# Kernel optimization log

Hardware: AMD Instinct MI355X
Metric: run time of the kernel (lower is better)

The kernel has to match this reference:

```python
import jax, jax.numpy as jnp
import numpy as np


def setup_inputs() -> dict:
    key = jax.random.key(0)
    k1, k2, k3, k4, k5 = jax.random.split(key, 5)
    B, S, d_in, d_out, r = 4, 2048, 4096, 4096, 16
    x = jax.random.normal(k1, (B, S, d_in), dtype=jnp.float32)
    weight = jax.random.normal(k2, (d_out, d_in), dtype=jnp.float32) * 0.02
    bias = jax.random.normal(k3, (d_out,), dtype=jnp.float32) * 0.02
    lora_A = jax.random.normal(k4, (r, d_in), dtype=jnp.float32) * 0.02
    lora_B = jax.random.normal(k5, (d_out, r), dtype=jnp.float32) * 0.02
    return {"x": x, "weight": weight, "bias": bias, "lora_A": lora_A, "lora_B": lora_B}


def reference(x, weight, bias, lora_A, lora_B):
    # weight_delta = lora_B @ lora_A  -> [out, in]; adjusted = W + delta
    # out = x @ adjusted.T + bias  (F.linear semantics)
    adjusted = weight + lora_B @ lora_A  # [out, in]
    return jnp.einsum('bsi,oi->bso', x, adjusted) + bias
```

## Files before the change

### kernel.cpp

```cpp
#include <hip/hip_runtime.h>
#include <hip/hip_bf16.h>
#include <stdint.h>

typedef int   intx4  __attribute__((ext_vector_type(4)));
typedef float floatx4 __attribute__((ext_vector_type(4)));

#define BM  256
#define BN  256
#define BKB 128

__device__ __forceinline__ void gload_lds16(const void* g, void* l) {
    auto* gp = reinterpret_cast<const __attribute__((address_space(1))) uint32_t*>(
        reinterpret_cast<uintptr_t>(g));
    auto* lp = reinterpret_cast<__attribute__((address_space(3))) uint32_t*>(
        reinterpret_cast<uintptr_t>(l));
    __builtin_amdgcn_global_load_lds(gp, lp, 16, 0, 0);
}

__global__ void quant_fused(const float* __restrict__ x, const float* __restrict__ W,
                            const float* __restrict__ lA, const float* __restrict__ lB,
                            int8_t* __restrict__ xq, int8_t* __restrict__ wq,
                            float* __restrict__ sx, float* __restrict__ sw,
                            long Mrows, int N, int K, int r) {
    __shared__ float red[4][4];
    const int tid = threadIdx.x;
    const int wv  = tid >> 6;
    const long b = blockIdx.x;

    if (b < Mrows) {
        const long row = b;
        const float* xr = x + (size_t)row * K;
        float4 v[4];
        float am = 0.f;
#pragma unroll
        for (int i = 0; i < 4; ++i) {
            v[i] = ((const float4*)xr)[i * 256 + tid];
            am = fmaxf(am, fmaxf(fmaxf(fabsf(v[i].x), fabsf(v[i].y)),
                                 fmaxf(fabsf(v[i].z), fabsf(v[i].w))));
        }
#pragma unroll
        for (int off = 32; off; off >>= 1) am = fmaxf(am, __shfl_xor(am, off));
        if ((tid & 63) == 0) red[0][wv] = am;
        __syncthreads();
        am = fmaxf(fmaxf(red[0][0], red[0][1]), fmaxf(red[0][2], red[0][3]));
        const float inv = am > 0.f ? 127.0f / am : 0.f;
        if (tid == 0) sx[row] = am > 0.f ? am / 127.0f : 0.f;
        int8_t* dst = xq + (size_t)row * K;
#pragma unroll
        for (int i = 0; i < 4; ++i) {
            int q0 = min(127, max(-127, (int)rintf(v[i].x * inv)));
            int q1 = min(127, max(-127, (int)rintf(v[i].y * inv)));
            int q2 = min(127, max(-127, (int)rintf(v[i].z * inv)));
            int q3 = min(127, max(-127, (int)rintf(v[i].w * inv)));
            int packed = (q0 & 255) | ((q1 & 255) << 8) | ((q2 & 255) << 16) | (q3 << 24);
            *(int*)(dst + ((size_t)(i * 256 + tid)) * 4) = packed;
        }
    } else {
        const long w0 = (b - Mrows) * 4;
        float4 v[4][4];
#pragma unroll
        for (int rr = 0; rr < 4; ++rr) {
            const float* wr = W + (size_t)(w0 + rr) * K;
#pragma unroll
            for (int i = 0; i < 4; ++i)
                v[rr][i] = ((const float4*)wr)[i * 256 + tid];
        }
        for (int j = 0; j < r; ++j) {
            const float* ar = lA + (size_t)j * K;
            float b0 = lB[(w0 + 0) * r + j];
            float b1 = lB[(w0 + 1) * r + j];
            float b2 = lB[(w0 + 2) * r + j];
            float b3 = lB[(w0 + 3) * r + j];
#pragma unroll
            for (int i = 0; i < 4; ++i) {
                float4 a = ((const float4*)ar)[i * 256 + tid];
                v[0][i].x += b0 * a.x; v[0][i].y += b0 * a.y; v[0][i].z += b0 * a.z; v[0][i].w += b0 * a.w;
                v[1][i].x += b1 * a.x; v[1][i].y += b1 * a.y; v[1][i].z += b1 * a.z; v[1][i].w += b1 * a.w;
                v[2][i].x += b2 * a.x; v[2][i].y += b2 * a.y; v[2][i].z += b2 * a.z; v[2][i].w += b2 * a.w;
                v[3][i].x += b3 * a.x; v[3][i].y += b3 * a.y; v[3][i].z += b3 * a.z; v[3][i].w += b3 * a.w;
            }
        }
#pragma unroll
        for (int rr = 0; rr < 4; ++rr) {
            float a = 0.f;
#pragma unroll
            for (int i = 0; i < 4; ++i)
                a = fmaxf(a, fmaxf(fmaxf(fabsf(v[rr][i].x), fabsf(v[rr][i].y)),
                                   fmaxf(fabsf(v[rr][i].z), fabsf(v[rr][i].w))));
#pragma unroll
            for (int off = 32; off; off >>= 1) a = fmaxf(a, __shfl_xor(a, off));
            if ((tid & 63) == 0) red[rr][wv] = a;
        }
        __syncthreads();
#pragma unroll
        for (int rr = 0; rr < 4; ++rr) {
            float a = fmaxf(fmaxf(red[rr][0], red[rr][1]), fmaxf(red[rr][2], red[rr][3]));
            const float inv = a > 0.f ? 127.0f / a : 0.f;
            if (tid == 0) sw[w0 + rr] = a > 0.f ? a / 127.0f : 0.f;
            int8_t* dst = wq + (size_t)(w0 + rr) * K;
#pragma unroll
            for (int i = 0; i < 4; ++i) {
                int q0 = min(127, max(-127, (int)rintf(v[rr][i].x * inv)));
                int q1 = min(127, max(-127, (int)rintf(v[rr][i].y * inv)));
                int q2 = min(127, max(-127, (int)rintf(v[rr][i].z * inv)));
                int q3 = min(127, max(-127, (int)rintf(v[rr][i].w * inv)));
                int packed = (q0 & 255) | ((q1 & 255) << 8) | ((q2 & 255) << 16) | (q3 << 24);
                *(int*)(dst + ((size_t)(i * 256 + tid)) * 4) = packed;
            }
        }
    }
}

__global__ __launch_bounds__(512, 2)
void gemm_i8d(const int8_t* __restrict__ A,
              const int8_t* __restrict__ B,
              const float* __restrict__ bias,
              const float* __restrict__ sx, const float* __restrict__ sw,
              float* __restrict__ C,
              int M, int N, int K) {
    __shared__ __align__(16) int8_t lds[2][2][BM * BKB];

    const int nbn = N / BN;
    const int nwg = gridDim.x;
    int bid = blockIdx.x;
    int swz = bid;
    if ((nwg & 7) == 0) swz = (bid & 7) * (nwg >> 3) + (bid >> 3);
    const int bm = swz / nbn, bn = swz % nbn;

    const int th   = threadIdx.x;
    const int lane = th & 63;
    const int wid  = th >> 6;
    const int wm = wid >> 2;
    const int wn = wid & 3;
    const int lr = lane & 15;
    const int kg = lane >> 4;

    const int8_t* gA = A + (size_t)(bm * BM) * K;
    const int8_t* gB = B + (size_t)(bn * BN) * K;
    const int NT = K / BKB;

    intx4 acc[8][4];
#pragma unroll
    for (int m = 0; m < 8; ++m)
#pragma unroll
        for (int n = 0; n < 4; ++n)
            acc[m][n] = (intx4){0, 0, 0, 0};

    const int trow = th >> 3;
    const int tgr  = (th & 7) ^ (trow & 7);

    auto stageA = [&](int dbuf, int mh, int k0) {
#pragma unroll
        for (int g = 0; g < 2; ++g) {
            int p = g * 128 + mh * 64 + trow;
            gload_lds16(gA + (size_t)p * K + k0 + tgr * 16,
                        &lds[dbuf][0][(mh * 128 + g * 64) * BKB + th * 16]);
        }
    };
    auto stageB = [&](int dbuf, int nh, int k0) {
#pragma unroll
        for (int g = 0; g < 2; ++g) {
            int rest = g * 64 + trow;
            int p = (rest >> 5) * 64 + nh * 32 + (rest & 31);
            gload_lds16(gB + (size_t)p * K + k0 + tgr * 16,
                        &lds[dbuf][1][(nh * 128 + g * 64) * BKB + th * 16]);
        }
    };

    auto ldA = [&](const int8_t* base, int mh, int mp, int kk) -> intx4 {
        int l = mh * 128 + wm * 64 + mp * 16 + lr;
        int c = ((kk << 2) | kg) ^ (lr & 7);
        return *(const intx4*)(base + l * BKB + c * 16);
    };
    auto ldB = [&](const int8_t* base, int nh, int np, int kk) -> intx4 {
        int l = nh * 128 + wn * 32 + np * 16 + lr;
        int c = ((kk << 2) | kg) ^ (lr & 7);
        return *(const intx4*)(base + l * BKB + c * 16);
    };

    stageA(0, 0, 0); stageB(0, 0, 0); stageB(0, 1, 0); stageA(0, 1, 0);
    asm volatile("s_waitcnt vmcnt(0)" ::: "memory");
    asm volatile("s_barrier" ::: "memory");

    for (int t = 0; t < NT; ++t) {
        const int8_t* Ab = &lds[t & 1][0][0];
        const int8_t* Bb = &lds[t & 1][1][0];
        const int nb = (t + 1) & 1;

        if (t + 1 < NT) {
            const int k1 = (t + 1) * BKB;
            stageA(nb, 0, k1);
            stageB(nb, 0, k1);
            stageB(nb, 1, k1);
            stageA(nb, 1, k1);
        }

        intx4 af[4][2], af2[4][2], b0[2][2], b1[2][2];
#pragma unroll
        for (int mp = 0; mp < 4; ++mp)
#pragma unroll
            for (int kk = 0; kk < 2; ++kk)
                af[mp][kk] = ldA(Ab, 0, mp, kk);
#pragma unroll
        for (int np = 0; np < 2; ++np)
#pragma unroll
            for (int kk = 0; kk < 2; ++kk)
                b0[np][kk] = ldB(Bb, 0, np, kk);
#pragma unroll
        for (int np = 0; np < 2; ++np)
#pragma unroll
            for (int kk = 0; kk < 2; ++kk)
                b1[np][kk] = ldB(Bb, 1, np, kk);
#pragma unroll
        for (int mp = 0; mp < 4; ++mp)
#pragma unroll
            for (int kk = 0; kk < 2; ++kk)
                af2[mp][kk] = ldA(Ab, 1, mp, kk);

        __builtin_amdgcn_s_setprio(1);
#pragma unroll
        for (int mp = 0; mp < 4; ++mp)
#pragma unroll
            for (int np = 0; np < 2; ++np)
#pragma unroll
                for (int kk = 0; kk < 2; ++kk)
                    acc[mp][np] = __builtin_amdgcn_mfma_i32_16x16x64_i8(
                        af[mp][kk], b0[np][kk], acc[mp][np], 0, 0, 0);
#pragma unroll
        for (int mp = 0; mp < 4; ++mp)
#pragma unroll
            for (int np = 0; np < 2; ++np)
#pragma unroll
                for (int kk = 0; kk < 2; ++kk)
                    acc[mp][2 + np] = __builtin_amdgcn_mfma_i32_16x16x64_i8(
                        af[mp][kk], b1[np][kk], acc[mp][2 + np], 0, 0, 0);
#pragma unroll
        for (int mp = 0; mp < 4; ++mp)
#pragma unroll
            for (int np = 0; np < 2; ++np)
#pragma unroll
                for (int kk = 0; kk < 2; ++kk)
                    acc[4 + mp][np] = __builtin_amdgcn_mfma_i32_16x16x64_i8(
                        af2[mp][kk], b0[np][kk], acc[4 + mp][np], 0, 0, 0);
#pragma unroll
        for (int mp = 0; mp < 4; ++mp)
#pragma unroll
            for (int np = 0; np < 2; ++np)
#pragma unroll
                for (int kk = 0; kk < 2; ++kk)
                    acc[4 + mp][2 + np] = __builtin_amdgcn_mfma_i32_16x16x64_i8(
                        af2[mp][kk], b1[np][kk], acc[4 + mp][2 + np], 0, 0, 0);
        __builtin_amdgcn_s_setprio(0);

        asm volatile("s_waitcnt vmcnt(0)" ::: "memory");
        asm volatile("s_barrier" ::: "memory");
    }

    const int crow = bm * BM + wm * 128;
    const int ccol = bn * BN + wn * 64;
#pragma unroll
    for (int n = 0; n < 4; ++n) {
        int col = ccol + n * 16 + lr;
        float bv  = bias[col];
        float swc = sw[col];
#pragma unroll
        for (int m = 0; m < 8; ++m) {
            int row0 = crow + m * 16 + kg * 4;
            float4 s4 = *(const float4*)&sx[row0];
            C[(size_t)(row0 + 0) * N + col] = (float)acc[m][n][0] * (s4.x * swc) + bv;
            C[(size_t)(row0 + 1) * N + col] = (float)acc[m][n][1] * (s4.y * swc) + bv;
            C[(size_t)(row0 + 2) * N + col] = (float)acc[m][n][2] * (s4.z * swc) + bv;
            C[(size_t)(row0 + 3) * N + col] = (float)acc[m][n][3] * (s4.w * swc) + bv;
        }
    }
}

__global__ void xa_kernel(const float* __restrict__ x, const float* __restrict__ lA,
                          float* __restrict__ xa, long M, int K, int r) {
    long idx = (long)blockIdx.x * blockDim.x + threadIdx.x;
    long total = M * r;
    if (idx >= total) return;
    long m = idx / r; int j = (int)(idx % r);
    const float* xr = x + m * (long)K;
    const float* ar = lA + (size_t)j * K;
    float s = 0.f;
    for (int k = 0; k < K; k += 4) {
        float4 xv = *(const float4*)&xr[k];
        float4 av = *(const float4*)&ar[k];
        s += xv.x * av.x + xv.y * av.y + xv.z * av.z + xv.w * av.w;
    }
    xa[idx] = s;
}

__global__ void naive_out(const float* __restrict__ x, const float* __restrict__ W,
                          const float* __restrict__ bias, const float* __restrict__ xa,
                          const float* __restrict__ lB, float* __restrict__ out,
                          long M, int N, int K, int r) {
    long idx = (long)blockIdx.x * blockDim.x + threadIdx.x;
    long total = M * (long)N;
    if (idx >= total) return;
    long m = idx / N; int n = (int)(idx % N);
    const float* xr = x + m * (long)K;
    const float* wr = W + (size_t)n * K;
    float s = bias[n];
    for (int k = 0; k < K; k += 4) {
        float4 xv = *(const float4*)&xr[k];
        float4 wv = *(const float4*)&wr[k];
        s += xv.x * wv.x + xv.y * wv.y + xv.z * wv.z + xv.w * wv.w;
    }
    const float* xar = xa + m * r;
    const float* br  = lB + (size_t)n * r;
    for (int j = 0; j < r; ++j) s += xar[j] * br[j];
    out[idx] = s;
}

extern "C" void kernel_launch(void* const* d_in, const int* in_sizes, int n_in,
                              void* d_out, int out_size, void* d_ws, size_t ws_size,
                              hipStream_t stream) {
    const float* x    = (const float*)d_in[0];
    const float* W    = (const float*)d_in[1];
    const float* bias = (const float*)d_in[2];
    const float* lA   = (const float*)d_in[3];
    const float* lB   = (const float*)d_in[4];
    float* out = (float*)d_out;

    const int  N  = in_sizes[2];
    const int  Kd = in_sizes[1] / N;
    const int  r  = in_sizes[4] / N;
    const long M  = (long)in_sizes[0] / Kd;

    size_t xq_bytes = (size_t)M * Kd;
    size_t wq_bytes = (size_t)N * Kd;
    size_t sx_bytes = (size_t)M * sizeof(float);
    size_t sw_bytes = (size_t)N * sizeof(float);

    if (ws_size >= xq_bytes + wq_bytes + sx_bytes + sw_bytes &&
        (M % BM) == 0 && (N % BN) == 0 && (N % 4) == 0 &&
        Kd == 4096 && (Kd / BKB) >= 2) {
        int8_t* xq = (int8_t*)d_ws;
        int8_t* wq = (int8_t*)d_ws + xq_bytes;
        float*  sx = (float*)((char*)d_ws + xq_bytes + wq_bytes);
        float*  sw = sx + M;

        quant_fused<<<(int)(M + N / 4), 256, 0, stream>>>(x, W, lA, lB, xq, wq, sx, sw,
                                                          M, N, Kd, r);

        int grid = (int)(M / BM) * (N / BN);
        gemm_i8d<<<grid, 512, 0, stream>>>(xq, wq, bias, sx, sw, out, (int)M, N, Kd);
    } else {
        float* xa = (float*)d_ws;
        long total_xa = M * (long)r;
        int blk_xa = (int)((total_xa + 255) / 256);
        xa_kernel<<<blk_xa, 256, 0, stream>>>(x, lA, xa, M, Kd, r);
        long total_o = M * (long)N;
        int blk_o = (int)((total_o + 255) / 256);
        naive_out<<<blk_o, 256, 0, stream>>>(x, W, bias, xa, lB, out, M, N, Kd, r);
    }
}
```

Baseline: 195.5 us.

## Use 4 waves with 128x128 warp tiles in int8 GEMM

Restructures the int8 GEMM block from 8 waves (each 128x64) to 4 waves (each 128x128), doubling per-wave accumulators to 8x8 MFMA tiles and simplifying staging into one loop per operand. This raises MFMA-to-LDS-read ratio per wave and cuts LDS fragment traffic, at the cost of far more registers (256 acc VGPRs plus fragments), 1 block per CU occupancy, and fewer threads issuing global loads, which weakens latency hiding.

```diff
diff --git a/kernel.cpp b/kernel.cpp
--- a/kernel.cpp
+++ b/kernel.cpp
@@ -111,8 +111,8 @@
     }
 }
 
-__global__ __launch_bounds__(512, 2)
-void gemm_i8d(const int8_t* __restrict__ A,
+__global__ __launch_bounds__(256, 1)
+void gemm_i8w(const int8_t* __restrict__ A,
               const int8_t* __restrict__ B,
               const float* __restrict__ bias,
               const float* __restrict__ sx, const float* __restrict__ sw,
@@ -130,8 +130,8 @@
     const int th   = threadIdx.x;
     const int lane = th & 63;
     const int wid  = th >> 6;
-    const int wm = wid >> 2;
-    const int wn = wid & 3;
+    const int wm = wid >> 1;
+    const int wn = wid & 1;
     const int lr = lane & 15;
     const int kg = lane >> 4;
 
@@ -139,46 +139,38 @@
     const int8_t* gB = B + (size_t)(bn * BN) * K;
     const int NT = K / BKB;
 
-    intx4 acc[8][4];
+    intx4 acc[8][8];
 #pragma unroll
     for (int m = 0; m < 8; ++m)
 #pragma unroll
-        for (int n = 0; n < 4; ++n)
+        for (int n = 0; n < 8; ++n)
             acc[m][n] = (intx4){0, 0, 0, 0};
 
-    const int trow = th >> 3;
-    const int tgr  = (th & 7) ^ (trow & 7);
-
-    auto stageA = [&](int dbuf, int mh, int k0) {
-#pragma unroll
-        for (int g = 0; g < 2; ++g) {
-            int p = g * 128 + mh * 64 + trow;
-            gload_lds16(gA + (size_t)p * K + k0 + tgr * 16,
-                        &lds[dbuf][0][(mh * 128 + g * 64) * BKB + th * 16]);
+    const int srow8 = th >> 3;
+    const int tgr   = (th & 7) ^ (srow8 & 7);
+
+    auto stage = [&](int dbuf, int ab, const int8_t* gbase, int k0) {
+#pragma unroll
+        for (int g = 0; g < 8; ++g) {
+            int l = g * 32 + srow8;
+            gload_lds16(gbase + (size_t)l * K + k0 + tgr * 16,
+                        &lds[dbuf][ab][(size_t)g * 4096 + (size_t)th * 16]);
         }
     };
-    auto stageB = [&](int dbuf, int nh, int k0) {
-#pragma unroll
-        for (int g = 0; g < 2; ++g) {
-            int rest = g * 64 + trow;
-            int p = (rest >> 5) * 64 + nh * 32 + (rest & 31);
-            gload_lds16(gB + (size_t)p * K + k0 + tgr * 16,
-                        &lds[dbuf][1][(nh * 128 + g * 64) * BKB + th * 16]);
-        }
-    };
-
-    auto ldA = [&](const int8_t* base, int mh, int mp, int kk) -> intx4 {
-        int l = mh * 128 + wm * 64 + mp * 16 + lr;
+
+    auto ldA = [&](const int8_t* base, int mp, int kk) -> intx4 {
+        int l = wm * 128 + mp * 16 + lr;
         int c = ((kk << 2) | kg) ^ (lr & 7);
         return *(const intx4*)(base + l * BKB + c * 16);
     };
-    auto ldB = [&](const int8_t* base, int nh, int np, int kk) -> intx4 {
-        int l = nh * 128 + wn * 32 + np * 16 + lr;
+    auto ldB = [&](const int8_t* base, int np, int kk) -> intx4 {
+        int l = wn * 128 + np * 16 + lr;
         int c = ((kk << 2) | kg) ^ (lr & 7);
         return *(const intx4*)(base + l * BKB + c * 16);
     };
 
-    stageA(0, 0, 0); stageB(0, 0, 0); stageB(0, 1, 0); stageA(0, 1, 0);
+    stage(0, 0, gA, 0);
+    stage(0, 1, gB, 0);
     asm volatile("s_waitcnt vmcnt(0)" ::: "memory");
     asm volatile("s_barrier" ::: "memory");
 
@@ -189,67 +181,31 @@
 
         if (t + 1 < NT) {
             const int k1 = (t + 1) * BKB;
-            stageA(nb, 0, k1);
-            stageB(nb, 0, k1);
-            stageB(nb, 1, k1);
-            stageA(nb, 1, k1);
-        }
-
-        intx4 af[4][2], af2[4][2], b0[2][2], b1[2][2];
-#pragma unroll
-        for (int mp = 0; mp < 4; ++mp)
+            stage(nb, 0, gA, k1);
+            stage(nb, 1, gB, k1);
+        }
+
+        intx4 af[8][2], bf[8][2];
+#pragma unroll
+        for (int mp = 0; mp < 8; ++mp)
 #pragma unroll
             for (int kk = 0; kk < 2; ++kk)
-                af[mp][kk] = ldA(Ab, 0, mp, kk);
-#pragma unroll
-        for (int np = 0; np < 2; ++np)
+                af[mp][kk] = ldA(Ab, mp, kk);
+#pragma unroll
+        for (int np = 0; np < 8; ++np)
 #pragma unroll
             for (int kk = 0; kk < 2; ++kk)
-                b0[np][kk] = ldB(Bb, 0, np, kk);
-#pragma unroll
-        for (int np = 0; np < 2; ++np)
-#pragma unroll
-            for (int kk = 0; kk < 2; ++kk)
-                b1[np][kk] = ldB(Bb, 1, np, kk);
-#pragma unroll
-        for (int mp = 0; mp < 4; ++mp)
-#pragma unroll
-            for (int kk = 0; kk < 2; ++kk)
-                af2[mp][kk] = ldA(Ab, 1, mp, kk);
+                bf[np][kk] = ldB(Bb, np, kk);
 
         __builtin_amdgcn_s_setprio(1);
 #pragma unroll
-        for (int mp = 0; mp < 4; ++mp)
-#pragma unroll
-            for (int np = 0; np < 2; ++np)
+        for (int mp = 0; mp < 8; ++mp)
+#pragma unroll
+            for (int np = 0; np < 8; ++np)
 #pragma unroll
                 for (int kk = 0; kk < 2; ++kk)
                     acc[mp][np] = __builtin_amdgcn_mfma_i32_16x16x64_i8(
-                        af[mp][kk], b0[np][kk], acc[mp][np], 0, 0, 0);
-#pragma unroll
-        for (int mp = 0; mp < 4; ++mp)
-#pragma unroll
-            for (int np = 0; np < 2; ++np)
-#pragma unroll
-                for (int kk = 0; kk < 2; ++kk)
-                    acc[mp][2 + np] = __builtin_amdgcn_mfma_i32_16x16x64_i8(
-                        af[mp][kk], b1[np][kk], acc[mp][2 + np], 0, 0, 0);
-#pragma unroll
-        for (int mp = 0; mp < 4; ++mp)
-#pragma unroll
-            for (int np = 0; np < 2; ++np)
-#pragma unroll
-                for (int kk = 0; kk < 2; ++kk)
-                    acc[4 + mp][np] = __builtin_amdgcn_mfma_i32_16x16x64_i8(
-                        af2[mp][kk], b0[np][kk], acc[4 + mp][np], 0, 0, 0);
-#pragma unroll
-        for (int mp = 0; mp < 4; ++mp)
-#pragma unroll
-            for (int np = 0; np < 2; ++np)
-#pragma unroll
-                for (int kk = 0; kk < 2; ++kk)
-                    acc[4 + mp][2 + np] = __builtin_amdgcn_mfma_i32_16x16x64_i8(
-                        af2[mp][kk], b1[np][kk], acc[4 + mp][2 + np], 0, 0, 0);
+                        af[mp][kk], bf[np][kk], acc[mp][np], 0, 0, 0);
         __builtin_amdgcn_s_setprio(0);
 
         asm volatile("s_waitcnt vmcnt(0)" ::: "memory");
@@ -257,9 +213,9 @@
     }
 
     const int crow = bm * BM + wm * 128;
-    const int ccol = bn * BN + wn * 64;
-#pragma unroll
-    for (int n = 0; n < 4; ++n) {
+    const int ccol = bn * BN + wn * 128;
+#pragma unroll
+    for (int n = 0; n < 8; ++n) {
         int col = ccol + n * 16 + lr;
         float bv  = bias[col];
         float swc = sw[col];
@@ -346,7 +302,7 @@
                                                           M, N, Kd, r);
 
         int grid = (int)(M / BM) * (N / BN);
-        gemm_i8d<<<grid, 512, 0, stream>>>(xq, wq, bias, sx, sw, out, (int)M, N, Kd);
+        gemm_i8w<<<grid, 256, 0, stream>>>(xq, wq, bias, sx, sw, out, (int)M, N, Kd);
     } else {
         float* xa = (float*)d_ws;
         long total_xa = M * (long)r;
```

Result: slower. 208.8 us (+6.8%).
